# Optimization experiments

Measured on AMD Instinct MI355X. Metric: run time of the kernel, lower is better.

The kernel has to match this reference:

```python
import jax, jax.numpy as jnp
import numpy as np

N_HEADS = 16


def _apply_rope(x, cos, sin):
    # x: (B, T, H, hd); cos/sin: (max_len, hd//2)
    B, T, H, hd = x.shape
    c = cos[:T][None, :, None, :]  # (1, T, 1, hd//2)
    s = sin[:T][None, :, None, :]
    x1 = x[..., 0::2]
    x2 = x[..., 1::2]
    y1 = x1 * c - x2 * s
    y2 = x1 * s + x2 * c
    return jnp.stack((y1, y2), axis=-1).reshape(B, T, H, hd)


def _precompute_rope(head_dim, max_len):
    theta = 10000.0
    inv = 1.0 / theta ** (np.arange(0, head_dim, 2, dtype=np.float32) / head_dim)
    t = np.arange(max_len, dtype=np.float32)
    freqs = np.outer(t, inv)
    return jnp.asarray(np.cos(freqs)), jnp.asarray(np.sin(freqs))


def setup_inputs() -> dict:
    key = jax.random.key(0)
    k1, k2, k3 = jax.random.split(key, 3)
    B, T, C = 4, 2048, 2048
    hd = C // N_HEADS
    x = jax.random.normal(k1, (B, T, C), dtype=jnp.float32)
    w_attn = jax.random.normal(k2, (C, 3 * C), dtype=jnp.float32) * (C ** -0.5)
    w_proj = jax.random.normal(k3, (C, C), dtype=jnp.float32) * (C ** -0.5)
    rope_cos, rope_sin = _precompute_rope(hd, T)
    return {"x": x, "w_attn": w_attn, "w_proj": w_proj,
            "rope_cos": rope_cos, "rope_sin": rope_sin}


def reference(x, w_attn, w_proj, rope_cos, rope_sin):
    B, T, C = x.shape
    H = N_HEADS
    hd = C // H
    qkv = x @ w_attn  # (B, T, 3C)
    q, k, v = jnp.split(qkv, 3, axis=2)
    q = q.reshape(B, T, H, hd)
    k = k.reshape(B, T, H, hd)
    v = v.reshape(B, T, H, hd)
    q = _apply_rope(q, rope_cos, rope_sin)
    k = _apply_rope(k, rope_cos, rope_sin)
    scale = 1.0 / jnp.sqrt(jnp.asarray(hd, dtype=x.dtype))
    scores = jnp.einsum('bqhd,bkhd->bhqk', q, k) * scale  # (B, H, T, T)
    causal = jnp.tril(jnp.ones((T, T), dtype=bool))
    scores = jnp.where(causal[None, None], scores, jnp.finfo(scores.dtype).min)
    attn = jax.nn.softmax(scores, axis=-1)
    y = jnp.einsum('bhqk,bkhd->bqhd', attn, v).reshape(B, T, C)
    return y @ w_proj
```

## Files before the change

kernel.cpp:

```cpp
#include <hip/hip_runtime.h>
#include <cstdint>
#include <cstddef>

#define DEVI __device__ __forceinline__

typedef __attribute__((ext_vector_type(8))) short bf16x8;
typedef __attribute__((ext_vector_type(4))) float f32x4;

DEVI unsigned short f2bf(float f) {
  unsigned int u = __float_as_uint(f);
  u += 0x7fffu + ((u >> 16) & 1u);
  return (unsigned short)(u >> 16);
}
DEVI float bf2f(unsigned int us) { return __uint_as_float(us << 16); }

DEVI void gld_lds16(const void* g, void* l) {
  __builtin_amdgcn_global_load_lds(
      (const __attribute__((address_space(1))) void*)g,
      (__attribute__((address_space(3))) void*)l, 16, 0, 0);
}

__global__ __launch_bounds__(256) void k_conv(const float* __restrict__ in,
                                              short* __restrict__ out, int n4) {
  int i = blockIdx.x * 256 + threadIdx.x;
  if (i >= n4) return;
  float4 v = reinterpret_cast<const float4*>(in)[i];
  uint2 o;
  o.x = (unsigned)f2bf(v.x) | ((unsigned)f2bf(v.y) << 16);
  o.y = (unsigned)f2bf(v.z) | ((unsigned)f2bf(v.w) << 16);
  reinterpret_cast<uint2*>(out)[i] = o;
}

__global__ __launch_bounds__(256) void k_transpose(const float* __restrict__ in,
                                                   short* __restrict__ out,
                                                   int R, int Cc) {
  __shared__ short tile[64][66];
  int tcols = Cc >> 6;
  int tb = blockIdx.x % tcols;
  int rb = blockIdx.x / tcols;
  int tid = threadIdx.x;
#pragma unroll
  for (int rep = 0; rep < 16; ++rep) {
    int idx = rep * 256 + tid;
    int r = idx >> 6, c = idx & 63;
    tile[r][c] = (short)f2bf(in[(size_t)(rb * 64 + r) * Cc + tb * 64 + c]);
  }
  __syncthreads();
#pragma unroll
  for (int rep = 0; rep < 16; ++rep) {
    int idx = rep * 256 + tid;
    int r = idx >> 6, c = idx & 63;
    out[(size_t)(tb * 64 + r) * R + rb * 64 + c] = tile[c][r];
  }
}

template <int MODE, typename OutT>
__global__ __launch_bounds__(512, 2) void k_gemm9(const short* __restrict__ A,
                                                  const short* __restrict__ BT,
                                                  OutT* __restrict__ C,
                                                  int M, int N, int K,
                                                  const float* __restrict__ cosb,
                                                  const float* __restrict__ sinb,
                                                  short* __restrict__ Qr,
                                                  short* __restrict__ Kr,
                                                  short* __restrict__ VT) {
  __shared__ short sA[2][256 * 64];
  __shared__ short sB[2][256 * 64];
  const int tid = threadIdx.x;
  const int wv = tid >> 6, lane = tid & 63;
  const int l16 = lane & 15, lhi = lane >> 4;
  const int wr = wv >> 2, wc = wv & 3;
  const int bm = blockIdx.x * 256, bn = blockIdx.y * 256;
  const int NT = K >> 6;
  const int lr8 = lane >> 3, lg8 = lane & 7;

  auto stageA = [&](int half, int kt, int b) {
#pragma unroll
    for (int j = 0; j < 2; ++j) {
      int row0 = j * 128 + wv * 8 + half * 64;
      int row = row0 + lr8;
      int g = lg8 ^ lr8;
      gld_lds16(A + (size_t)(bm + row) * K + kt + g * 8, &sA[b][row0 * 64]);
    }
  };
  auto stageB = [&](int half, int kt, int b) {
#pragma unroll
    for (int j = 0; j < 2; ++j) {
      int ri0 = j * 64 + wv * 8;
      int row0 = (ri0 >> 5) * 64 + half * 32 + (ri0 & 31);
      int row = row0 + lr8;
      int g = lg8 ^ lr8;
      gld_lds16(BT + (size_t)(bn + row) * K + kt + g * 8, &sB[b][row0 * 64]);
    }
  };

  f32x4 acc[8][4] = {};
  bf16x8 af03[4][2], af47[4][2], bf01[2][2], bf23[2][2];

#define RD_A(DST, MB, BUF)                                                     \
  _Pragma("unroll") for (int m = 0; m < 4; ++m)                                \
      _Pragma("unroll") for (int ks = 0; ks < 2; ++ks) {                       \
    int row = wr * 128 + ((MB) + m) * 16 + l16;                                \
    DST[m][ks] = *(const bf16x8*)&(BUF)[row * 64 +                             \
                                        (((ks * 4 + lhi) ^ (row & 7)) << 3)];  \
  }
#define RD_B(DST, NB, BUF)                                                     \
  _Pragma("unroll") for (int n = 0; n < 2; ++n)                                \
      _Pragma("unroll") for (int ks = 0; ks < 2; ++ks) {                       \
    int row = wc * 64 + ((NB) + n) * 16 + l16;                                 \
    DST[n][ks] = *(const bf16x8*)&(BUF)[row * 64 +                             \
                                        (((ks * 4 + lhi) ^ (row & 7)) << 3)];  \
  }
#define MMA_Q(AF, BF, MO, NO)                                                  \
  __builtin_amdgcn_s_setprio(1);                                               \
  _Pragma("unroll") for (int m = 0; m < 4; ++m)                                \
      _Pragma("unroll") for (int n = 0; n < 2; ++n)                            \
          _Pragma("unroll") for (int ks = 0; ks < 2; ++ks)                     \
              acc[(MO) + m][(NO) + n] = __builtin_amdgcn_mfma_f32_16x16x32_bf16(\
                  AF[m][ks], BF[n][ks], acc[(MO) + m][(NO) + n], 0, 0, 0);     \
  __builtin_amdgcn_s_setprio(0);
#define GATE(NN)                                                               \
  __builtin_amdgcn_sched_barrier(0);                                           \
  asm volatile("s_waitcnt vmcnt(" #NN ")" ::: "memory");                       \
  __builtin_amdgcn_s_barrier();                                                \
  asm volatile("s_waitcnt lgkmcnt(0)" ::: "memory");                           \
  __builtin_amdgcn_sched_barrier(0);

  stageA(0, 0, 0); stageB(0, 0, 0); stageB(1, 0, 0); stageA(1, 0, 0);
  asm volatile("s_waitcnt vmcnt(0)" ::: "memory");
  __builtin_amdgcn_s_barrier();

  for (int t = 0; t < NT; ++t) {
    const int cur = t & 1;
    const int kt1 = (t + 1) * 64;
    const bool pf = (t + 1 < NT);
    const short* bufA = sA[cur];
    const short* bufB = sB[cur];
    RD_A(af03, 0, bufA);
    if (pf) stageA(0, kt1, cur ^ 1);
    if (pf) { GATE(6); } else { GATE(4); }
    if (t) { MMA_Q(af47, bf23, 4, 2); }
    __builtin_amdgcn_s_barrier();
    RD_B(bf01, 0, bufB);
    if (pf) stageB(0, kt1, cur ^ 1);
    if (pf) { GATE(6); } else { GATE(2); }
    MMA_Q(af03, bf01, 0, 0);
    __builtin_amdgcn_s_barrier();
    RD_B(bf23, 2, bufB);
    if (pf) stageB(1, kt1, cur ^ 1);
    if (pf) { GATE(6); } else { GATE(0); }
    MMA_Q(af03, bf23, 0, 2);
    __builtin_amdgcn_s_barrier();
    RD_A(af47, 4, bufA);
    if (pf) stageA(1, kt1, cur ^ 1);
    GATE(6);
    MMA_Q(af47, bf01, 4, 0);
    __builtin_amdgcn_s_barrier();
  }
  MMA_Q(af47, bf23, 4, 2);
#undef RD_A
#undef RD_B
#undef MMA_Q
#undef GATE

  if constexpr (MODE == 1) {
#pragma unroll
    for (int m = 0; m < 8; ++m) {
#pragma unroll
      for (int n = 0; n < 4; ++n) {
        int col = bn + wc * 64 + n * 16 + l16;
#pragma unroll
        for (int r = 0; r < 4; ++r) {
          int row = bm + wr * 128 + m * 16 + lhi * 4 + r;
          C[(size_t)row * N + col] = acc[m][n][r];
        }
      }
    }
  } else {
    const int part = bn >> 11;
    const float kC = 0.08838834764831845f * 1.44269504088896340f;
    if (part < 2) {
      const float qs = (part == 0) ? kC : 1.0f;
      short* dst = (part == 0) ? Qr : Kr;
#pragma unroll
      for (int m = 0; m < 8; ++m) {
#pragma unroll
        for (int n = 0; n < 4; ++n) {
          int colm = (bn & 2047) + wc * 64 + n * 16 + l16;
          int h = colm >> 7, d = colm & 127;
          int p2 = d >> 1;
          bool ev = (d & 1) == 0;
#pragma unroll
          for (int r = 0; r < 4; ++r) {
            int row = bm + wr * 128 + m * 16 + lhi * 4 + r;
            int b = row >> 11, t = row & 2047;
            float c = cosb[t * 64 + p2];
            float s = sinb[t * 64 + p2];
            float x = acc[m][n][r];
            float xp = __shfl_xor(x, 1);
            float y = ev ? (x * c - xp * s) : (xp * s + x * c);
            dst[((size_t)(b * 16 + h) * 2048 + t) * 128 + d] =
                (short)f2bf(y * qs);
          }
        }
      }
    } else {
#pragma unroll
      for (int m = 0; m < 8; ++m) {
#pragma unroll
        for (int n = 0; n < 4; ++n) {
          int colm = (bn & 2047) + wc * 64 + n * 16 + l16;
          int h = colm >> 7, d = colm & 127;
#pragma unroll
          for (int r = 0; r < 4; ++r) {
            int row = bm + wr * 128 + m * 16 + lhi * 4 + r;
            int b = row >> 11, t = row & 2047;
            VT[((size_t)(b * 16 + h) * 128 + d) * 2048 + t] =
                (short)f2bf(acc[m][n][r]);
          }
        }
      }
    }
  }
}

__global__ __launch_bounds__(256) void k_attn(const short* __restrict__ Qr,
                                              const short* __restrict__ Kr,
                                              const short* __restrict__ VT,
                                              short* __restrict__ Y) {
  __shared__ short sK[2][64 * 128];
  __shared__ short sVT[2][128 * 64];
  __shared__ short sP[4][16 * 64];
  const int tid = threadIdx.x, wv = tid >> 6, lane = tid & 63;
  const int l8r = lane >> 3, l8c = lane & 7, l16 = lane & 15, lhi = lane >> 4;
  const int bid = blockIdx.x;
  const int pair = bid & 15, bh = bid >> 4;
  const size_t base = (size_t)bh * 2048 * 128;
  const int b = bh >> 4, h = bh & 15;

  const short ob = (short)0x3F80;
  const bf16x8 ones = {ob, ob, ob, ob, ob, ob, ob, ob};

  auto stage = [&](int kv0, int buf) {
#pragma unroll
    for (int rr = 0; rr < 4; ++rr) {
      int ch = rr * 4 + wv;
      {
        int row = ch * 4 + lhi;
        int wch = l16 ^ (row & 7);
        gld_lds16(Kr + base + (size_t)(kv0 + row) * 128 + wch * 8,
                  &sK[buf][ch * 512]);
      }
      {
        int drow = ch * 8 + l8r;
        int wch = l8c ^ (drow & 7);
        gld_lds16(VT + base + (size_t)drow * 2048 + kv0 + wch * 8,
                  &sVT[buf][ch * 512]);
      }
    }
  };

  for (int half = 0; half < 2; ++half) {
    const int qt = half ? 31 - pair : pair;
    const int q0 = qt * 64;
    const int nt = qt + 1;

    bf16x8 qf[4];
    const int qrow = q0 + wv * 16 + l16;
#pragma unroll
    for (int ks = 0; ks < 4; ++ks)
      qf[ks] = *reinterpret_cast<const bf16x8*>(Qr + base + (size_t)qrow * 128 +
                                                ks * 32 + lhi * 8);

    f32x4 acc_o[8] = {};
    f32x4 acc_l = {};
    float m_run[4];
#pragma unroll
    for (int r = 0; r < 4; ++r) m_run[r] = -1e30f;

    stage(0, 0);
    __syncthreads();

    for (int it = 0; it < nt; ++it) {
      const int cur = it & 1;
      if (it + 1 < nt) stage((it + 1) * 64, cur ^ 1);

      f32x4 sacc[4] = {};
      __builtin_amdgcn_s_setprio(1);
#pragma unroll
      for (int cf = 0; cf < 4; ++cf) {
        int krow = cf * 16 + l16;
#pragma unroll
        for (int ks = 0; ks < 4; ++ks) {
          int e = krow * 128 + ks * 32 + lhi * 8;
          bf16x8 kf = *reinterpret_cast<const bf16x8*>(
              &sK[cur][e ^ ((krow & 7) << 3)]);
          sacc[cf] = __builtin_amdgcn_mfma_f32_16x16x32_bf16(qf[ks], kf,
                                                             sacc[cf], 0, 0, 0);
        }
      }
      __builtin_amdgcn_s_setprio(0);

      if (it == nt - 1) {
#pragma unroll
        for (int cf = 0; cf < 4; ++cf) {
          int col = cf * 16 + l16;
#pragma unroll
          for (int r = 0; r < 4; ++r)
            if (col > wv * 16 + lhi * 4 + r) sacc[cf][r] = -3e38f;
        }
      }

      bool exceed = false;
#pragma unroll
      for (int cf = 0; cf < 4; ++cf)
#pragma unroll
        for (int r = 0; r < 4; ++r)
          exceed |= (sacc[cf][r] > m_run[r] + 8.f);

      if (__any(exceed)) {
        float resc[4];
#pragma unroll
        for (int r = 0; r < 4; ++r) {
          float mx = fmaxf(fmaxf(sacc[0][r], sacc[1][r]),
                           fmaxf(sacc[2][r], sacc[3][r]));
          mx = fmaxf(mx, __shfl_xor(mx, 1));
          mx = fmaxf(mx, __shfl_xor(mx, 2));
          mx = fmaxf(mx, __shfl_xor(mx, 4));
          mx = fmaxf(mx, __shfl_xor(mx, 8));
          float mnew = fmaxf(m_run[r], mx);
          resc[r] = exp2f(m_run[r] - mnew);
          m_run[r] = mnew;
        }
#pragma unroll
        for (int df = 0; df < 8; ++df)
#pragma unroll
          for (int r = 0; r < 4; ++r) acc_o[df][r] *= resc[r];
#pragma unroll
        for (int r = 0; r < 4; ++r) acc_l[r] *= resc[r];
      }

#pragma unroll
      for (int cf = 0; cf < 4; ++cf)
#pragma unroll
        for (int r = 0; r < 4; ++r) {
          float p = exp2f(sacc[cf][r] - m_run[r]);
          int prow = lhi * 4 + r;
          int e = prow * 64 + cf * 16 + l16;
          sP[wv][e ^ ((prow & 7) << 3)] = (short)f2bf(p);
        }

      __builtin_amdgcn_s_setprio(1);
#pragma unroll
      for (int kk = 0; kk < 2; ++kk) {
        int e = l16 * 64 + kk * 32 + lhi * 8;
        bf16x8 pa = *reinterpret_cast<const bf16x8*>(
            &sP[wv][e ^ ((l16 & 7) << 3)]);
        acc_l = __builtin_amdgcn_mfma_f32_16x16x32_bf16(pa, ones, acc_l, 0, 0, 0);
#pragma unroll
        for (int df = 0; df < 8; ++df) {
          int vrow = df * 16 + l16;
          int ev = vrow * 64 + kk * 32 + lhi * 8;
          bf16x8 vb = *reinterpret_cast<const bf16x8*>(
              &sVT[cur][ev ^ ((vrow & 7) << 3)]);
          acc_o[df] = __builtin_amdgcn_mfma_f32_16x16x32_bf16(pa, vb,
                                                              acc_o[df], 0, 0, 0);
        }
      }
      __builtin_amdgcn_s_setprio(0);
      __syncthreads();
    }

    float inv[4];
#pragma unroll
    for (int r = 0; r < 4; ++r) inv[r] = 1.f / acc_l[r];
#pragma unroll
    for (int df = 0; df < 8; ++df) {
      int col = h * 128 + df * 16 + l16;
#pragma unroll
      for (int r = 0; r < 4; ++r) {
        int row = q0 + wv * 16 + lhi * 4 + r;
        Y[((size_t)b * 2048 + row) * 2048 + col] =
            (short)f2bf(acc_o[df][r] * inv[r]);
      }
    }
  }
}

extern "C" void kernel_launch(void* const* d_in, const int* in_sizes, int n_in,
                              void* d_out, int out_size, void* d_ws, size_t ws_size,
                              hipStream_t stream) {
  const float* x        = (const float*)d_in[0];
  const float* w_attn   = (const float*)d_in[1];
  const float* w_proj   = (const float*)d_in[2];
  const float* rope_cos = (const float*)d_in[3];
  const float* rope_sin = (const float*)d_in[4];

  char* ws = (char*)d_ws;
  short* xbf    = (short*)(ws);
  short* wattnT = (short*)(ws + 33554432ull);
  short* wprojT = (short*)(ws + 58720256ull);
  short* Y      = (short*)(ws + 67108864ull);
  short* Qr     = (short*)(ws + 167772160ull);
  short* Kr     = (short*)(ws + 201326592ull);
  short* VT     = (short*)(ws + 234881024ull);

  k_conv<<<16384, 256, 0, stream>>>(x, xbf, 4194304);
  k_transpose<<<3072, 256, 0, stream>>>(w_attn, wattnT, 2048, 6144);
  k_transpose<<<1024, 256, 0, stream>>>(w_proj, wprojT, 2048, 2048);
  k_gemm9<2, short><<<dim3(32, 24), 512, 0, stream>>>(
      xbf, wattnT, (short*)nullptr, 8192, 6144, 2048,
      rope_cos, rope_sin, Qr, Kr, VT);
  k_attn<<<1024, 256, 0, stream>>>(Qr, Kr, VT, Y);
  k_gemm9<1, float><<<dim3(32, 8), 512, 0, stream>>>(
      Y, wprojT, (float*)d_out, 8192, 2048, 2048,
      nullptr, nullptr, nullptr, nullptr, nullptr);
}
```

Baseline: 473.9 us.

## Merge prep kernels into one launch and relax GEMM pipeline wait gates

The conversion kernel and the two weight-transpose kernels are merged into a single launch that dispatches on block index, removing two kernel launches and their gaps. In the GEMM main loop, the combined vmcnt-wait, barrier and lgkmcnt(0) gates are replaced. Only two of the four phases now wait on global loads (vmcnt(4)), and the other phases use a bare barrier with no explicit LDS-read wait. This is meant to reduce stalls around the MFMA phases, but it depends on the compiler inserting the needed lgkmcnt waits before fragment use, and the changed vmcnt accounting could expose ordering hazards on the double buffer.

Result: faster. 464.3 us (-2.0%).

```diff
diff --git a/kernel.cpp b/kernel.cpp
--- a/kernel.cpp
+++ b/kernel.cpp
@@ -20,25 +20,33 @@
       (__attribute__((address_space(3))) void*)l, 16, 0, 0);
 }
 
-__global__ __launch_bounds__(256) void k_conv(const float* __restrict__ in,
-                                              short* __restrict__ out, int n4) {
-  int i = blockIdx.x * 256 + threadIdx.x;
-  if (i >= n4) return;
-  float4 v = reinterpret_cast<const float4*>(in)[i];
-  uint2 o;
-  o.x = (unsigned)f2bf(v.x) | ((unsigned)f2bf(v.y) << 16);
-  o.y = (unsigned)f2bf(v.z) | ((unsigned)f2bf(v.w) << 16);
-  reinterpret_cast<uint2*>(out)[i] = o;
-}
-
-__global__ __launch_bounds__(256) void k_transpose(const float* __restrict__ in,
-                                                   short* __restrict__ out,
-                                                   int R, int Cc) {
+__global__ __launch_bounds__(256) void k_prep(const float* __restrict__ x,
+                                              short* __restrict__ xbf,
+                                              const float* __restrict__ w_attn,
+                                              short* __restrict__ wattnT,
+                                              const float* __restrict__ w_proj,
+                                              short* __restrict__ wprojT) {
+  const int bid = blockIdx.x, tid = threadIdx.x;
+  if (bid < 16384) {
+    int i = bid * 256 + tid;
+    float4 v = reinterpret_cast<const float4*>(x)[i];
+    uint2 o;
+    o.x = (unsigned)f2bf(v.x) | ((unsigned)f2bf(v.y) << 16);
+    o.y = (unsigned)f2bf(v.z) | ((unsigned)f2bf(v.w) << 16);
+    reinterpret_cast<uint2*>(xbf)[i] = o;
+    return;
+  }
   __shared__ short tile[64][66];
-  int tcols = Cc >> 6;
-  int tb = blockIdx.x % tcols;
-  int rb = blockIdx.x / tcols;
-  int tid = threadIdx.x;
+  const float* in;
+  short* out;
+  int R, Cc, tb, rb;
+  if (bid < 19456) {
+    in = w_attn; out = wattnT; R = 2048; Cc = 6144;
+    int t = bid - 16384; tb = t % 96; rb = t / 96;
+  } else {
+    in = w_proj; out = wprojT; R = 2048; Cc = 2048;
+    int t = bid - 19456; tb = t % 32; rb = t / 32;
+  }
 #pragma unroll
   for (int rep = 0; rep < 16; ++rep) {
     int idx = rep * 256 + tid;
@@ -55,15 +63,15 @@
 }
 
 template <int MODE, typename OutT>
-__global__ __launch_bounds__(512, 2) void k_gemm9(const short* __restrict__ A,
-                                                  const short* __restrict__ BT,
-                                                  OutT* __restrict__ C,
-                                                  int M, int N, int K,
-                                                  const float* __restrict__ cosb,
-                                                  const float* __restrict__ sinb,
-                                                  short* __restrict__ Qr,
-                                                  short* __restrict__ Kr,
-                                                  short* __restrict__ VT) {
+__global__ __launch_bounds__(512, 2) void k_gemm10(const short* __restrict__ A,
+                                                   const short* __restrict__ BT,
+                                                   OutT* __restrict__ C,
+                                                   int M, int N, int K,
+                                                   const float* __restrict__ cosb,
+                                                   const float* __restrict__ sinb,
+                                                   short* __restrict__ Qr,
+                                                   short* __restrict__ Kr,
+                                                   short* __restrict__ VT) {
   __shared__ short sA[2][256 * 64];
   __shared__ short sB[2][256 * 64];
   const int tid = threadIdx.x;
@@ -119,41 +127,45 @@
               acc[(MO) + m][(NO) + n] = __builtin_amdgcn_mfma_f32_16x16x32_bf16(\
                   AF[m][ks], BF[n][ks], acc[(MO) + m][(NO) + n], 0, 0, 0);     \
   __builtin_amdgcn_s_setprio(0);
-#define GATE(NN)                                                               \
-  __builtin_amdgcn_sched_barrier(0);                                           \
-  asm volatile("s_waitcnt vmcnt(" #NN ")" ::: "memory");                       \
-  __builtin_amdgcn_s_barrier();                                                \
-  asm volatile("s_waitcnt lgkmcnt(0)" ::: "memory");                           \
-  __builtin_amdgcn_sched_barrier(0);
 
   stageA(0, 0, 0); stageB(0, 0, 0); stageB(1, 0, 0); stageA(1, 0, 0);
   asm volatile("s_waitcnt vmcnt(0)" ::: "memory");
   __builtin_amdgcn_s_barrier();
 
   for (int t = 0; t < NT; ++t) {
-    const int cur = t & 1;
+    const int cur = t & 1, nxt = cur ^ 1;
     const int kt1 = (t + 1) * 64;
     const bool pf = (t + 1 < NT);
     const short* bufA = sA[cur];
     const short* bufB = sB[cur];
     RD_A(af03, 0, bufA);
-    if (pf) stageA(0, kt1, cur ^ 1);
-    if (pf) { GATE(6); } else { GATE(4); }
+    if (pf) stageA(0, kt1, nxt);
+    __builtin_amdgcn_s_barrier();
     if (t) { MMA_Q(af47, bf23, 4, 2); }
     __builtin_amdgcn_s_barrier();
     RD_B(bf01, 0, bufB);
-    if (pf) stageB(0, kt1, cur ^ 1);
-    if (pf) { GATE(6); } else { GATE(2); }
+    if (pf) {
+      stageB(0, kt1, nxt);
+      asm volatile("s_waitcnt vmcnt(4)" ::: "memory");
+    } else {
+      asm volatile("s_waitcnt vmcnt(0)" ::: "memory");
+    }
+    __builtin_amdgcn_s_barrier();
     MMA_Q(af03, bf01, 0, 0);
     __builtin_amdgcn_s_barrier();
     RD_B(bf23, 2, bufB);
-    if (pf) stageB(1, kt1, cur ^ 1);
-    if (pf) { GATE(6); } else { GATE(0); }
+    if (pf) stageB(1, kt1, nxt);
+    __builtin_amdgcn_s_barrier();
     MMA_Q(af03, bf23, 0, 2);
     __builtin_amdgcn_s_barrier();
     RD_A(af47, 4, bufA);
-    if (pf) stageA(1, kt1, cur ^ 1);
-    GATE(6);
+    if (pf) {
+      stageA(1, kt1, nxt);
+      asm volatile("s_waitcnt vmcnt(4)" ::: "memory");
+    } else {
+      asm volatile("s_waitcnt vmcnt(0)" ::: "memory");
+    }
+    __builtin_amdgcn_s_barrier();
     MMA_Q(af47, bf01, 4, 0);
     __builtin_amdgcn_s_barrier();
   }
@@ -161,7 +173,6 @@
 #undef RD_A
 #undef RD_B
 #undef MMA_Q
-#undef GATE
 
   if constexpr (MODE == 1) {
 #pragma unroll
@@ -405,14 +416,12 @@
   short* Kr     = (short*)(ws + 201326592ull);
   short* VT     = (short*)(ws + 234881024ull);
 
-  k_conv<<<16384, 256, 0, stream>>>(x, xbf, 4194304);
-  k_transpose<<<3072, 256, 0, stream>>>(w_attn, wattnT, 2048, 6144);
-  k_transpose<<<1024, 256, 0, stream>>>(w_proj, wprojT, 2048, 2048);
-  k_gemm9<2, short><<<dim3(32, 24), 512, 0, stream>>>(
+  k_prep<<<20480, 256, 0, stream>>>(x, xbf, w_attn, wattnT, w_proj, wprojT);
+  k_gemm10<2, short><<<dim3(32, 24), 512, 0, stream>>>(
       xbf, wattnT, (short*)nullptr, 8192, 6144, 2048,
       rope_cos, rope_sin, Qr, Kr, VT);
   k_attn<<<1024, 256, 0, stream>>>(Qr, Kr, VT, Y);
-  k_gemm9<1, float><<<dim3(32, 8), 512, 0, stream>>>(
+  k_gemm10<1, float><<<dim3(32, 8), 512, 0, stream>>>(
       Y, wprojT, (float*)d_out, 8192, 2048, 2048,
       nullptr, nullptr, nullptr, nullptr, nullptr);
 }
```
